# Performance work log

Measured on AMD Instinct MI355X. Metric: run time of the kernel, lower is better.

The kernel has to match this reference:

```python
import jax, jax.numpy as jnp
import numpy as np

DIM = 2048
N_HEADS = 16
KV_HEADS = 2
HEAD_DIM = DIM // N_HEADS
N_REP = N_HEADS // KV_HEADS
EPS = 1e-6


def rms_norm(x, weight):
    # norm over last dim in float32, cast back (inputs already fp32 here)
    xf = x.astype(jnp.float32)
    n = xf * jax.lax.rsqrt(jnp.mean(xf * xf, axis=-1, keepdims=True) + EPS)
    return (weight * n).astype(x.dtype)


def rotate_half(x):
    x1, x2 = jnp.split(x, 2, axis=-1)
    return jnp.concatenate((-x2, x1), axis=-1)


def apply_rotary(x, cos, sin):
    return x * cos + rotate_half(x) * sin


def setup_inputs() -> dict:
    key = jax.random.key(0)
    ks = jax.random.split(key, 8)
    B, S = 2, 2048
    x = jax.random.normal(ks[0], (B, S, DIM), dtype=jnp.float32)
    cos = jax.random.uniform(ks[1], (1, 1, S, HEAD_DIM), dtype=jnp.float32)
    sin = jax.random.uniform(ks[2], (1, 1, S, HEAD_DIM), dtype=jnp.float32)
    scale = 0.02
    wq = jax.random.normal(ks[3], (N_HEADS * HEAD_DIM, DIM), dtype=jnp.float32) * scale
    wk = jax.random.normal(ks[4], (KV_HEADS * HEAD_DIM, DIM), dtype=jnp.float32) * scale
    wv = jax.random.normal(ks[5], (KV_HEADS * HEAD_DIM, DIM), dtype=jnp.float32) * scale
    wo = jax.random.normal(ks[6], (DIM, N_HEADS * HEAD_DIM), dtype=jnp.float32) * scale
    q_gamma = jnp.ones((HEAD_DIM,), dtype=jnp.float32)
    k_gamma = jnp.ones((HEAD_DIM,), dtype=jnp.float32)
    return {"x": x, "cos": cos, "sin": sin, "wq": wq, "wk": wk, "wv": wv,
            "wo": wo, "q_gamma": q_gamma, "k_gamma": k_gamma,
            "signal_token_num": 256}


def reference(x, cos, sin, wq, wk, wv, wo, q_gamma, k_gamma, signal_token_num):
    B, S, D = x.shape
    p = signal_token_num
    # projections (Linear with no bias: x @ W.T)
    xq = (x @ wq.T).reshape(B, S, N_HEADS, HEAD_DIM)
    xk = (x @ wk.T).reshape(B, S, KV_HEADS, HEAD_DIM)
    xv = (x @ wv.T).reshape(B, S, KV_HEADS, HEAD_DIM)
    # QK RMSNorm per head_dim
    xq = rms_norm(xq, q_gamma)
    xk = rms_norm(xk, k_gamma)
    # repeat kv heads (GQA) then [B,H,S,hd]
    xk = jnp.repeat(xk, N_REP, axis=2)
    xv = jnp.repeat(xv, N_REP, axis=2)
    xq = xq.transpose(0, 2, 1, 3)
    xk = xk.transpose(0, 2, 1, 3)
    xv = xv.transpose(0, 2, 1, 3)
    # rotary: original applies identical cos/sin to [:p] and [p:] slices == full apply
    xq = apply_rotary(xq, cos, sin)
    xk = apply_rotary(xk, cos, sin)
    # causal mask with bidirectional prefix block [:p,:p]
    i = jnp.arange(S)[:, None]
    j = jnp.arange(S)[None, :]
    mask = (j <= i) | ((i < p) & (j < p))  # [S,S] bool
    scale = 1.0 / np.sqrt(HEAD_DIM)
    scores = jnp.einsum('bhqd,bhkd->bhqk', xq, xk) * scale
    scores = jnp.where(mask, scores, jnp.finfo(scores.dtype).min)
    attn = jax.nn.softmax(scores, axis=-1)
    out = jnp.einsum('bhqk,bhkd->bhqd', attn, xv)  # [B,H,S,hd]
    out = out.transpose(0, 2, 1, 3).reshape(B, S, N_HEADS * HEAD_DIM)
    return out @ wo.T
```

## Files before the change

### kernel.cpp

```cpp
#include <hip/hip_runtime.h>
#include <stdint.h>

#define S_LEN 2048
#define DIMM  2048
#define NH    16
#define NKV   2

typedef __attribute__((ext_vector_type(8)))  short s16x8;
typedef __attribute__((ext_vector_type(8)))  unsigned short u16x8;
typedef __attribute__((ext_vector_type(4)))  float f32x4;
typedef __attribute__((ext_vector_type(16))) float f32x16;
typedef __attribute__((ext_vector_type(4)))  unsigned int u32x4;

__device__ __forceinline__ unsigned short f2bf(float f){
  unsigned int u = __builtin_bit_cast(unsigned int, f);
  u += 0x7fffu + ((u >> 16) & 1u);
  return (unsigned short)(u >> 16);
}

__device__ __forceinline__ float bf2f(unsigned short u){
  return __builtin_bit_cast(float, ((unsigned int)u) << 16);
}

__device__ __forceinline__ unsigned int cvtpk(float lo, float hi){
  unsigned int r;
  asm("v_cvt_pk_bf16_f32 %0, %1, %2" : "=v"(r) : "v"(lo), "v"(hi));
  return r;
}

__device__ __forceinline__ void gload16(const void* g, void* l){
  __builtin_amdgcn_global_load_lds(
      (const __attribute__((address_space(1))) unsigned int*)g,
      (__attribute__((address_space(3))) unsigned int*)l, 16, 0, 0);
}

__global__ __launch_bounds__(256) void cvt_bf16(const float* __restrict__ src,
                                                unsigned short* __restrict__ dst, int n){
  int i = (blockIdx.x * 256 + threadIdx.x) * 8;
  if (i >= n) return;
  const float4* s4 = (const float4*)(src + i);
  float4 a = s4[0], b = s4[1];
  u16x8 o;
  o[0]=f2bf(a.x); o[1]=f2bf(a.y); o[2]=f2bf(a.z); o[3]=f2bf(a.w);
  o[4]=f2bf(b.x); o[5]=f2bf(b.y); o[6]=f2bf(b.z); o[7]=f2bf(b.w);
  *(u16x8*)(dst + i) = o;
}

template<bool OBF16>
__global__ __launch_bounds__(256) void gemm_bt(const unsigned short* __restrict__ A,
                                               const unsigned short* __restrict__ W,
                                               void* __restrict__ Cv,
                                               int M, int N, int K){
  __shared__ __attribute__((aligned(16))) unsigned short As[128*64];
  __shared__ __attribute__((aligned(16))) unsigned short Bs[128*64];
  const int t = threadIdx.x;
  const int lane = t & 63, wave = t >> 6;
  const int l15 = lane & 15, g = lane >> 4;
  const int lid = blockIdx.y * gridDim.x + blockIdx.x;
  const int cpx = (gridDim.x * gridDim.y) >> 3;
  const int swz = (lid & 7) * cpx + (lid >> 3);
  const int m0 = (swz / gridDim.x) * 128, n0 = (swz % gridDim.x) * 128;
  const int wm = (wave >> 1) * 64, wn = (wave & 1) * 64;
  const int srow = t >> 3, sdblk = t & 7;
  const long ldsoff = (long)(t >> 6) * 1024;
  f32x4 acc[4][4] = {};
  for (int k0 = 0; k0 < K; k0 += 64){
    __syncthreads();
    #pragma unroll
    for (int r = 0; r < 4; ++r){
      int row = r*32 + srow;
      int db  = sdblk ^ (row & 7);
      gload16(A + (long)(m0+row)*K + k0 + db*8, (char*)As + r*4096 + ldsoff);
    }
    #pragma unroll
    for (int r = 0; r < 4; ++r){
      int row = r*32 + srow;
      int db  = sdblk ^ (row & 7);
      gload16(W + (long)(n0+row)*K + k0 + db*8, (char*)Bs + r*4096 + ldsoff);
    }
    __syncthreads();
    s16x8 af[4][2], bfr[4][2];
    #pragma unroll
    for (int mi = 0; mi < 4; ++mi)
      #pragma unroll
      for (int kc = 0; kc < 2; ++kc){
        int row = wm + mi*16 + l15;
        int db = (kc*4 + g) ^ (row & 7);
        af[mi][kc] = *(const s16x8*)(As + row*64 + db*8);
      }
    #pragma unroll
    for (int ni = 0; ni < 4; ++ni)
      #pragma unroll
      for (int kc = 0; kc < 2; ++kc){
        int row = wn + ni*16 + l15;
        int db = (kc*4 + g) ^ (row & 7);
        bfr[ni][kc] = *(const s16x8*)(Bs + row*64 + db*8);
      }
    #pragma unroll
    for (int mi = 0; mi < 4; ++mi)
      #pragma unroll
      for (int ni = 0; ni < 4; ++ni)
        #pragma unroll
        for (int kc = 0; kc < 2; ++kc)
          acc[mi][ni] = __builtin_amdgcn_mfma_f32_16x16x32_bf16(af[mi][kc], bfr[ni][kc], acc[mi][ni], 0, 0, 0);
  }
  #pragma unroll
  for (int mi = 0; mi < 4; ++mi)
    #pragma unroll
    for (int ni = 0; ni < 4; ++ni)
      #pragma unroll
      for (int rg = 0; rg < 4; ++rg){
        int row = m0 + wm + mi*16 + g*4 + rg;
        int col = n0 + wn + ni*16 + l15;
        if (OBF16)
          ((unsigned short*)Cv)[(long)row*N + col] = f2bf(acc[mi][ni][rg]);
        else
          ((float*)Cv)[(long)row*N + col] = acc[mi][ni][rg];
      }
}

__global__ __launch_bounds__(256) void normrope(const unsigned short* __restrict__ qkv,
    const float* __restrict__ cosb, const float* __restrict__ sinb,
    const float* __restrict__ qg, const float* __restrict__ kg,
    unsigned short* __restrict__ q_attn, unsigned short* __restrict__ k_attn){
  int wave = threadIdx.x >> 6, lane = threadIdx.x & 63;
  int rid = blockIdx.x * 4 + wave;
  int d0 = lane * 2;
  const unsigned short* src; unsigned short* dst; const float* gm; float sc; int s;
  if (rid < 2*S_LEN*NH){
    int bs = rid >> 4, h = rid & 15;
    int b = bs >> 11; s = bs & 2047;
    src = qkv + (long)bs*2560 + h*128;
    dst = q_attn + ((long)(b*NH + h)*S_LEN + s)*128;
    gm = qg; sc = 0.08838834764831845f * 1.4426950408889634f;
  } else {
    int r2 = rid - 2*S_LEN*NH;
    int bs = r2 >> 1, kv = r2 & 1;
    int b = bs >> 11; s = bs & 2047;
    src = qkv + (long)bs*2560 + 2048 + kv*128;
    dst = k_attn + ((long)(b*NKV + kv)*S_LEN + s)*128;
    gm = kg; sc = 1.0f;
  }
  unsigned int xw = *(const unsigned int*)(src + d0);
  float x0 = bf2f((unsigned short)(xw & 0xffff));
  float x1 = bf2f((unsigned short)(xw >> 16));
  float ss = x0*x0 + x1*x1;
  #pragma unroll
  for (int m = 1; m < 64; m <<= 1) ss += __shfl_xor(ss, m);
  float r = rsqrtf(ss * (1.0f/128.0f) + 1e-6f);
  float2 gv = *(const float2*)(gm + d0);
  float n0 = x0 * r * gv.x, n1 = x1 * r * gv.y;
  float p0 = __shfl_xor(n0, 32), p1 = __shfl_xor(n1, 32);
  float sgn = (d0 < 64) ? -1.f : 1.f;
  float2 c  = *(const float2*)(cosb + (long)s*128 + d0);
  float2 sn = *(const float2*)(sinb + (long)s*128 + d0);
  float o0 = (n0*c.x + sgn*p0*sn.x) * sc;
  float o1 = (n1*c.y + sgn*p1*sn.y) * sc;
  unsigned int pk = (unsigned int)f2bf(o0) | ((unsigned int)f2bf(o1) << 16);
  *(unsigned int*)(dst + d0) = pk;
}

__global__ __launch_bounds__(256) void vtrans(const unsigned short* __restrict__ qkv,
                                              unsigned short* __restrict__ v_t){
  __shared__ __attribute__((aligned(16))) unsigned short lds[128*72];
  int bid = blockIdx.x;
  int s0 = (bid & 31) * 64;
  int kv = (bid >> 5) & 1;
  int b  = bid >> 6;
  int t = threadIdx.x;
  #pragma unroll
  for (int it = 0; it < 32; ++it){
    int idx = it*256 + t;
    int s = idx >> 7, d = idx & 127;
    lds[d*72 + s] = qkv[(long)(b*S_LEN + s0 + s)*2560 + 2304 + kv*128 + d];
  }
  __syncthreads();
  #pragma unroll
  for (int it = 0; it < 4; ++it){
    int c = it*256 + t;
    int d = c >> 3, s8 = c & 7;
    u16x8 vv = *(const u16x8*)(lds + d*72 + s8*8);
    *(u16x8*)(v_t + ((long)(b*NKV + kv)*128 + d)*S_LEN + s0 + s8*8) = vv;
  }
}

__global__ __launch_bounds__(256, 2) void attn_fwd(const unsigned short* __restrict__ q_attn,
    const unsigned short* __restrict__ k_attn, const unsigned short* __restrict__ v_t,
    unsigned short* __restrict__ attn_out, const int* __restrict__ pp){
  __shared__ __attribute__((aligned(16))) unsigned short Ks[2][64*128];
  const int p = pp[0];
  int bid = blockIdx.x;
  int qsb = 15 - (bid >> 5);
  int bh = bid & 31;
  int h = bh & 15, b = bh >> 4;
  int kvh = h >> 3;
  int t = threadIdx.x, wave = t >> 6, lane = t & 63;
  int l31 = lane & 31, hi = lane >> 5;
  int QS = qsb * 128;
  int qw0 = QS + wave*32;
  const int q = qw0 + l31;
  const unsigned short* qb = q_attn + ((long)(b*NH + h)*S_LEN + q)*128 + hi*8;
  s16x8 qf[8];
  #pragma unroll
  for (int m = 0; m < 8; ++m) qf[m] = *(const s16x8*)(qb + m*16);
  f32x16 O[4] = {};
  float mr = -3e38f, lr = 0.f;
  int kvend_w = (qw0 + 31 < p) ? ((p > qw0 + 32) ? p : qw0 + 32) : (qw0 + 32);
  int n_w = (kvend_w + 63) >> 6;
  int kvend_b = (QS + 127 < p) ? ((p > QS + 128) ? p : QS + 128) : (QS + 128);
  int n_blk = (kvend_b + 63) >> 6;
  const unsigned short* kb0 = k_attn + ((long)(b*NKV + kvh)*S_LEN)*128;
  const unsigned short* vb0 = v_t + ((long)(b*NKV + kvh)*128)*S_LEN;
  const int srow = t >> 4, sunit = t & 15;
  const long ldsoff = (long)wave * 1024;
  const unsigned short* vbase = vb0 + (long)l31*S_LEN + hi*8;

  #pragma unroll
  for (int r = 0; r < 4; ++r){
    int row = r*16 + srow;
    int un  = sunit ^ (row & 15);
    gload16(kb0 + (long)row*128 + un*8, (char*)Ks[0] + r*4096 + ldsoff);
  }
  __syncthreads();
  int buf = 0;

  #pragma unroll 1
  for (int ti = 0; ti < n_blk; ++ti){
    int j0 = ti * 64;
    bool act = ti < n_w;
    s16x8 vfA[2][4], vfB[2][4];
    if (act){
      #pragma unroll
      for (int dt = 0; dt < 2; ++dt)
        #pragma unroll
        for (int km = 0; km < 4; ++km)
          vfA[dt][km] = *(const s16x8*)(vbase + (long)dt*32*S_LEN + j0 + km*16);
    }
    if (ti + 1 < n_blk){
      const unsigned short* kb = kb0 + (long)(j0 + 64)*128;
      char* dst = (char*)Ks[buf^1] + ldsoff;
      #pragma unroll
      for (int r = 0; r < 4; ++r){
        int row = r*16 + srow;
        int un  = sunit ^ (row & 15);
        gload16(kb + (long)row*128 + un*8, dst + r*4096);
      }
    }
    if (act){
      const unsigned short* ksc = Ks[buf];
      f32x16 sa[2] = {};
      __builtin_amdgcn_s_setprio(1);
      #pragma unroll
      for (int kt = 0; kt < 2; ++kt){
        int row = kt*32 + l31;
        #pragma unroll
        for (int m = 0; m < 8; ++m){
          int un = (2*m + hi) ^ (row & 15);
          s16x8 kf = *(const s16x8*)(ksc + row*128 + un*8);
          sa[kt] = __builtin_amdgcn_mfma_f32_32x32x16_bf16(kf, qf[m], sa[kt], 0, 0, 0);
        }
      }
      __builtin_amdgcn_s_setprio(0);
      #pragma unroll
      for (int dt = 0; dt < 2; ++dt)
        #pragma unroll
        for (int km = 0; km < 4; ++km)
          vfB[dt][km] = *(const s16x8*)(vbase + (long)(dt+2)*32*S_LEN + j0 + km*16);
      float tm = -3e38f;
      bool full = (j0 + 63 <= qw0) || ((qw0 + 31 < p) && (j0 + 63 < p));
      if (full){
        #pragma unroll
        for (int kt = 0; kt < 2; ++kt)
          #pragma unroll
          for (int rg = 0; rg < 16; ++rg) tm = fmaxf(tm, sa[kt][rg]);
      } else {
        #pragma unroll
        for (int kt = 0; kt < 2; ++kt)
          #pragma unroll
          for (int rg = 0; rg < 16; ++rg){
            int j = j0 + kt*32 + (rg & 3) + 8*(rg >> 2) + 4*hi;
            bool ok = (j <= q) || ((q < p) && (j < p));
            float sv = ok ? sa[kt][rg] : -3e38f;
            sa[kt][rg] = sv;
            tm = fmaxf(tm, sv);
          }
      }
      tm = fmaxf(tm, __shfl_xor(tm, 32));
      if (!__all(tm <= mr + 8.0f)){
        float nm = fmaxf(mr, tm);
        float sfv = exp2f(mr - nm);
        mr = nm;
        lr *= sfv;
        float sfO[16];
        #pragma unroll
        for (int rg = 0; rg < 16; ++rg){
          int qr = (rg & 3) + 8*(rg >> 2) + 4*hi;
          sfO[rg] = __shfl(sfv, qr | (lane & 32));
        }
        #pragma unroll
        for (int dt = 0; dt < 4; ++dt)
          #pragma unroll
          for (int rg = 0; rg < 16; ++rg) O[dt][rg] *= sfO[rg];
      }
      float rs = 0.f;
      #pragma unroll
      for (int kt = 0; kt < 2; ++kt)
        #pragma unroll
        for (int rg = 0; rg < 16; ++rg){
          float e = exp2f(sa[kt][rg] - mr);
          sa[kt][rg] = e;
          rs += e;
        }
      rs += __shfl_xor(rs, 32);
      lr += rs;
      __builtin_amdgcn_s_setprio(1);
      #pragma unroll
      for (int km = 0; km < 4; ++km){
        int base = (km & 1) * 8;
        const f32x16& s = sa[km >> 1];
        unsigned int a0 = cvtpk(s[base+0], s[base+1]);
        unsigned int b0 = cvtpk(s[base+4], s[base+5]);
        asm("v_permlane32_swap_b32 %0, %1" : "+v"(a0), "+v"(b0));
        unsigned int a1 = cvtpk(s[base+2], s[base+3]);
        unsigned int b1 = cvtpk(s[base+6], s[base+7]);
        asm("v_permlane32_swap_b32 %0, %1" : "+v"(a1), "+v"(b1));
        u32x4 w; w[0] = a0; w[1] = a1; w[2] = b0; w[3] = b1;
        s16x8 pf = __builtin_bit_cast(s16x8, w);
        #pragma unroll
        for (int dt = 0; dt < 2; ++dt)
          O[dt] = __builtin_amdgcn_mfma_f32_32x32x16_bf16(pf, vfA[dt][km], O[dt], 0, 0, 0);
        #pragma unroll
        for (int dt = 2; dt < 4; ++dt)
          O[dt] = __builtin_amdgcn_mfma_f32_32x32x16_bf16(pf, vfB[dt-2][km], O[dt], 0, 0, 0);
      }
      __builtin_amdgcn_s_setprio(0);
    }
    __syncthreads();
    buf ^= 1;
  }
  float inv = 1.0f / lr;
  float invO[16];
  #pragma unroll
  for (int rg = 0; rg < 16; ++rg){
    int qr = (rg & 3) + 8*(rg >> 2) + 4*hi;
    invO[rg] = __shfl(inv, qr | (lane & 32));
  }
  #pragma unroll
  for (int dt = 0; dt < 4; ++dt)
    #pragma unroll
    for (int rg = 0; rg < 16; ++rg){
      int row = qw0 + (rg & 3) + 8*(rg >> 2) + 4*hi;
      int col = h*128 + dt*32 + l31;
      attn_out[(long)(b*S_LEN + row)*DIMM + col] = f2bf(O[dt][rg]*invO[rg]);
    }
}

extern "C" void kernel_launch(void* const* d_in, const int* in_sizes, int n_in,
                              void* d_out, int out_size, void* d_ws, size_t ws_size,
                              hipStream_t stream){
  const float* x    = (const float*)d_in[0];
  const float* cosb = (const float*)d_in[1];
  const float* sinb = (const float*)d_in[2];
  const float* wq   = (const float*)d_in[3];
  const float* wk   = (const float*)d_in[4];
  const float* wv   = (const float*)d_in[5];
  const float* wo   = (const float*)d_in[6];
  const float* qg   = (const float*)d_in[7];
  const float* kg   = (const float*)d_in[8];
  const int*   pp   = (const int*)d_in[9];

  char* ws = (char*)d_ws;
  unsigned short* xb    = (unsigned short*)(ws);
  unsigned short* wqkvb = (unsigned short*)(ws + 16777216);
  unsigned short* wob   = (unsigned short*)(ws + 27262976);
  unsigned short* qkvb  = (unsigned short*)(ws + 35651584);
  unsigned short* qat   = (unsigned short*)(ws + 77594624);
  unsigned short* kat   = (unsigned short*)(ws + 94371840);
  unsigned short* vt    = (unsigned short*)(ws + 96468992);
  unsigned short* aout  = (unsigned short*)(ws + 98566144);

  cvt_bf16<<<8388608/2048, 256, 0, stream>>>(x,  xb, 8388608);
  cvt_bf16<<<4194304/2048, 256, 0, stream>>>(wq, wqkvb, 4194304);
  cvt_bf16<<< 524288/2048, 256, 0, stream>>>(wk, wqkvb + 4194304, 524288);
  cvt_bf16<<< 524288/2048, 256, 0, stream>>>(wv, wqkvb + 4718592, 524288);
  cvt_bf16<<<4194304/2048, 256, 0, stream>>>(wo, wob, 4194304);

  gemm_bt<true><<<dim3(2560/128, 4096/128), 256, 0, stream>>>(xb, wqkvb, qkvb, 4096, 2560, 2048);
  normrope<<<73728/4, 256, 0, stream>>>(qkvb, cosb, sinb, qg, kg, qat, kat);
  vtrans<<<128, 256, 0, stream>>>(qkvb, vt);
  attn_fwd<<<512, 256, 0, stream>>>(qat, kat, vt, aout, pp);
  gemm_bt<false><<<dim3(2048/128, 4096/128), 256, 0, stream>>>(aout, wob, d_out, 4096, 2048, 2048);
}
```

Measured before the change: 253.1 us.

## Deepen attention K prefetch to two tiles and fuse fp32→bf16 conversion launches

The attention kernel grows its K shared-memory ring from 2 to 4 tiles. It prefetches two tiles ahead and issues a block barrier only after every other iteration, so global loads have longer to land and fewer synchronisations are paid. Separately, the five fp32-to-bf16 conversion launches are merged into one kernel that picks its source and destination by global thread index, removing launch overhead. The cost is double the LDS per attention block, which may lower occupancy, and a more delicate correctness argument for the halved barriers.

```diff
diff --git a/kernel.cpp b/kernel.cpp
--- a/kernel.cpp
+++ b/kernel.cpp
@@ -34,10 +34,19 @@
       (__attribute__((address_space(3))) unsigned int*)l, 16, 0, 0);
 }
 
-__global__ __launch_bounds__(256) void cvt_bf16(const float* __restrict__ src,
-                                                unsigned short* __restrict__ dst, int n){
-  int i = (blockIdx.x * 256 + threadIdx.x) * 8;
-  if (i >= n) return;
+__global__ __launch_bounds__(256) void cvt_all(const float* __restrict__ x,
+    const float* __restrict__ wq, const float* __restrict__ wk,
+    const float* __restrict__ wv, const float* __restrict__ wo,
+    unsigned short* __restrict__ xb, unsigned short* __restrict__ wqkvb,
+    unsigned short* __restrict__ wob){
+  long gid = (long)blockIdx.x * 256 + threadIdx.x;
+  const float* src; unsigned short* dst; long off;
+  if (gid < 1048576)      { src = x;  dst = xb;              off = gid; }
+  else if (gid < 1572864) { src = wq; dst = wqkvb;           off = gid - 1048576; }
+  else if (gid < 1638400) { src = wk; dst = wqkvb + 4194304; off = gid - 1572864; }
+  else if (gid < 1703936) { src = wv; dst = wqkvb + 4718592; off = gid - 1638400; }
+  else                    { src = wo; dst = wob;             off = gid - 1703936; }
+  long i = off * 8;
   const float4* s4 = (const float4*)(src + i);
   float4 a = s4[0], b = s4[1];
   u16x8 o;
@@ -187,7 +196,7 @@
 __global__ __launch_bounds__(256, 2) void attn_fwd(const unsigned short* __restrict__ q_attn,
     const unsigned short* __restrict__ k_attn, const unsigned short* __restrict__ v_t,
     unsigned short* __restrict__ attn_out, const int* __restrict__ pp){
-  __shared__ __attribute__((aligned(16))) unsigned short Ks[2][64*128];
+  __shared__ __attribute__((aligned(16))) unsigned short Ks[4][64*128];
   const int p = pp[0];
   int bid = blockIdx.x;
   int qsb = 15 - (bid >> 5);
@@ -216,13 +225,16 @@
   const unsigned short* vbase = vb0 + (long)l31*S_LEN + hi*8;
 
   #pragma unroll
-  for (int r = 0; r < 4; ++r){
-    int row = r*16 + srow;
-    int un  = sunit ^ (row & 15);
-    gload16(kb0 + (long)row*128 + un*8, (char*)Ks[0] + r*4096 + ldsoff);
+  for (int pt = 0; pt < 2; ++pt){
+    const unsigned short* kb = kb0 + (long)(pt*64)*128;
+    #pragma unroll
+    for (int r = 0; r < 4; ++r){
+      int row = r*16 + srow;
+      int un  = sunit ^ (row & 15);
+      gload16(kb + (long)row*128 + un*8, (char*)Ks[pt] + r*4096 + ldsoff);
+    }
   }
   __syncthreads();
-  int buf = 0;
 
   #pragma unroll 1
   for (int ti = 0; ti < n_blk; ++ti){
@@ -236,9 +248,9 @@
         for (int km = 0; km < 4; ++km)
           vfA[dt][km] = *(const s16x8*)(vbase + (long)dt*32*S_LEN + j0 + km*16);
     }
-    if (ti + 1 < n_blk){
-      const unsigned short* kb = kb0 + (long)(j0 + 64)*128;
-      char* dst = (char*)Ks[buf^1] + ldsoff;
+    if (ti + 2 < n_blk){
+      const unsigned short* kb = kb0 + (long)(j0 + 128)*128;
+      char* dst = (char*)Ks[(ti+2)&3] + ldsoff;
       #pragma unroll
       for (int r = 0; r < 4; ++r){
         int row = r*16 + srow;
@@ -247,7 +259,7 @@
       }
     }
     if (act){
-      const unsigned short* ksc = Ks[buf];
+      const unsigned short* ksc = Ks[ti & 3];
       f32x16 sa[2] = {};
       __builtin_amdgcn_s_setprio(1);
       #pragma unroll
@@ -335,8 +347,7 @@
       }
       __builtin_amdgcn_s_setprio(0);
     }
-    __syncthreads();
-    buf ^= 1;
+    if (ti & 1) __syncthreads();
   }
   float inv = 1.0f / lr;
   float invO[16];
@@ -379,11 +390,7 @@
   unsigned short* vt    = (unsigned short*)(ws + 96468992);
   unsigned short* aout  = (unsigned short*)(ws + 98566144);
 
-  cvt_bf16<<<8388608/2048, 256, 0, stream>>>(x,  xb, 8388608);
-  cvt_bf16<<<4194304/2048, 256, 0, stream>>>(wq, wqkvb, 4194304);
-  cvt_bf16<<< 524288/2048, 256, 0, stream>>>(wk, wqkvb + 4194304, 524288);
-  cvt_bf16<<< 524288/2048, 256, 0, stream>>>(wv, wqkvb + 4718592, 524288);
-  cvt_bf16<<<4194304/2048, 256, 0, stream>>>(wo, wob, 4194304);
+  cvt_all<<<8704, 256, 0, stream>>>(x, wq, wk, wv, wo, xb, wqkvb, wob);
 
   gemm_bt<true><<<dim3(2560/128, 4096/128), 256, 0, stream>>>(xb, wqkvb, qkvb, 4096, 2560, 2048);
   normrope<<<73728/4, 256, 0, stream>>>(qkvb, cosb, sinb, qg, kg, qat, kat);
```

After: 244.4 us. -3.4%, faster.
